# Optimization experiments

Hardware: AMD Instinct MI355X
Metric: run time of the kernel (lower is better)

The kernel has to match this reference:

```python
import jax, jax.numpy as jnp
import numpy as np

# ---- static skeleton topology (20 edges, humanoid: spine + 2 arms + 2 legs) ----
EDGES = [(0,1),(1,2),(2,3),(3,4),(3,5),(5,6),(6,7),(7,8),(3,9),(9,10),(10,11),(11,12),
         (0,13),(13,14),(14,15),(15,16),(0,17),(17,18),(18,19),(19,20)]
SKELETON_DIST = 2
IN_PER_J, OUT_PER_J = 64, 128
KSIZE, PAD, STRIDE = 15, 7, 2
BATCH, T = 8, 4096


def _calc_edge_mat(edges):
    n = len(edges)
    INF = 100000
    m = np.full((n, n), INF, dtype=np.int64)
    np.fill_diagonal(m, 0)
    for i, a in enumerate(edges):
        for j, b in enumerate(edges):
            if a[0] in b or a[1] in b:
                m[i, j] = min(m[i, j], 1)
    for k in range(n):  # Floyd-Warshall on tiny static graph
        m = np.minimum(m, m[:, k:k+1] + m[k:k+1, :])
    return m


def _find_neighbor(edges, d):
    m = _calc_edge_mat(edges)
    n = len(edges)
    neigh = [[j for j in range(n) if m[i, j] <= d] for i in range(n)]
    global_part = list(neigh[0])
    for i in global_part:
        neigh[i].append(n)  # virtual global edge index n
    neigh.append(global_part)
    return neigh


def _build_mask(neigh, in_pj, out_pj, k):
    J = len(neigh)
    mask = np.zeros((J * out_pj, J * in_pj, k), dtype=np.float32)
    for i, nb in enumerate(neigh):
        for j in nb:
            mask[i*out_pj:(i+1)*out_pj, j*in_pj:(j+1)*in_pj, :] = 1.0
    return mask


def _build_pool_weight(edges, cpe):
    degree = [0] * 100
    for e in edges:
        degree[e[0]] += 1
        degree[e[1]] += 1
    seq_list = []
    def find_seq(j, seq):
        if degree[j] > 2 and j != 0:
            seq_list.append(seq); seq = []
        if degree[j] == 1:
            seq_list.append(seq); return
        for idx, e in enumerate(edges):
            if e[0] == j:
                find_seq(e[1], seq + [idx])
    find_seq(0, [])
    pooling = []
    for seq in seq_list:
        seq = list(seq)
        if len(seq) % 2 == 1:
            pooling.append([seq[0]]); seq = seq[1:]
        for i in range(0, len(seq), 2):
            pooling.append([seq[i], seq[i+1]])
    edge_num = len(edges) + 1
    pooling.append([edge_num - 1])
    W = np.zeros((len(pooling) * cpe, edge_num * cpe), dtype=np.float32)
    for i, pair in enumerate(pooling):
        for j in pair:
            for c in range(cpe):
                W[i*cpe + c, j*cpe + c] = 1.0 / len(pair)
    return W


def setup_inputs() -> dict:
    key = jax.random.key(0)
    k1, k2, k3 = jax.random.split(key, 3)
    J = len(EDGES) + 1  # 21 (edges + virtual global)
    in_c, out_c = J * IN_PER_J, J * OUT_PER_J  # 1344, 2688
    neigh = _find_neighbor(EDGES, SKELETON_DIST)
    mask = jnp.asarray(_build_mask(neigh, IN_PER_J, OUT_PER_J, KSIZE))
    pool_w = jnp.asarray(_build_pool_weight(EDGES, out_c // J))
    x = jax.random.normal(k1, (BATCH, in_c, T), dtype=jnp.float32)
    weight = jax.random.normal(k2, (out_c, in_c, KSIZE), dtype=jnp.float32) * 0.02
    bias = jax.random.normal(k3, (out_c,), dtype=jnp.float32) * 0.01
    return {"x": x, "weight": weight, "bias": bias, "mask": mask, "pool_w": pool_w}


def reference(x, weight, bias, mask, pool_w):
    # SkeletonConv: per-joint neighbor mask applied to dense conv1d weights
    w = weight * mask  # [out_c, in_c, K]
    xp = jnp.pad(x, ((0, 0), (0, 0), (PAD, PAD)), mode='reflect')
    y = jax.lax.conv_general_dilated(
        xp, w, window_strides=(STRIDE,), padding='VALID',
        dimension_numbers=('NCH', 'OIH', 'NCH'))
    y = y + bias[None, :, None]  # [B, out_c, T//2]
    # SkeletonPool: mean over graph-defined edge groups via matmul
    p = jnp.einsum('pc,bct->bpt', pool_w, y)
    # LeakyReLU activation as in the layer stack
    return jax.nn.leaky_relu(p, negative_slope=0.2)
```

## Files before the change

kernel.cpp:

```cpp
#include <hip/hip_runtime.h>
#include <cstdint>
#include <cstddef>

typedef unsigned short u16;
typedef unsigned int   u32;

typedef __bf16 bf16x8 __attribute__((ext_vector_type(8)));
typedef float  f32x4  __attribute__((ext_vector_type(4)));

#define AS1C(p) ((const __attribute__((address_space(1))) void*)(p))
#define AS3(p)  ((__attribute__((address_space(3))) void*)(p))

__constant__ int d_slot_jb[85] = {
  0,1,2,12,13,16,17,20,
  0,1,2,3,4,5,8,9,12,16,20,
  1,2,3,4,5,8,9,
  1,2,3,4,5,6,7,8,9,
  4,5,6,7,
  1,2,3,4,5,8,9,10,11,
  8,9,10,11,
  0,1,12,13,14,15,16,17,20,
  12,13,14,15,
  0,1,12,13,16,17,18,19,20,
  16,17,18,19,
  0,1,2,12,13,16,17
};
__constant__ int   d_gs0[12]    = {0,8,19,26,35,39,48,52,61,65,74,78};
__constant__ int   d_gnb[12]    = {8,11,7,9,4,9,4,9,4,9,4,7};
__constant__ int   d_gj0[12]    = {0,1,3,4,6,8,10,12,14,16,18,20};
__constant__ int   d_gj1[12]    = {-1,2,-1,5,7,9,11,13,15,17,19,-1};
__constant__ float d_gscale[12] = {1.f,0.5f,1.f,0.5f,0.5f,0.5f,0.5f,0.5f,0.5f,0.5f,0.5f,1.f};
__constant__ int   d_sched[12]  = {1,3,5,7,9,0,2,11,4,6,8,10};

static __device__ __forceinline__ u16 f2bf(float f) {
  union { float f; u32 u; } v; v.f = f;
  u32 r = v.u + 0x7fffu + ((v.u >> 16) & 1u);
  return (u16)(r >> 16);
}

__global__ void prep_x(const float* __restrict__ x, u16* __restrict__ xp) {
  int gid = blockIdx.x * 256 + threadIdx.x;
  if (gid >= 8 * 1344 * 514) return;
  int pc  = gid % 514;
  int row = gid / 514;
  int p   = pc * 8;
  const float* xr = x + (size_t)row * 4096;
  u16 v[8];
#pragma unroll
  for (int e = 0; e < 8; ++e) {
    int j = p + e - 7;
    j = j < 0 ? -j : (j > 4095 ? 8190 - j : j);
    v[e] = f2bf(xr[j]);
  }
  *(uint4*)(xp + (size_t)row * 4112 + p) = *(const uint4*)v;
}

__global__ void prep_w(const float* __restrict__ wt, const float* __restrict__ msk,
                       u16* __restrict__ apk) {
  int gid = blockIdx.x * 256 + threadIdx.x;
  if (gid >= 85 * 8192) return;
  int u   = gid >> 13;
  int rem = gid & 8191;
  int m   = rem >> 6;
  int c   = rem & 63;
  int g = 11;
#pragma unroll
  for (int gg = 0; gg < 11; ++gg)
    if (u >= d_gs0[gg] && u < d_gs0[gg + 1]) g = gg;
  int jb = d_slot_jb[u];
  int j0 = d_gj0[g], j1 = d_gj1[g];
  float sc = d_gscale[g];
  float m0 = msk[((size_t)(j0 * 128) * 1344 + jb * 64) * 15];
  float m1 = (j1 >= 0) ? msk[((size_t)(j1 * 128) * 1344 + jb * 64) * 15] : 0.f;
  const float* w0 = wt + ((size_t)(j0 * 128 + m) * 1344 + jb * 64 + c) * 15;
  const float* w1 = (j1 >= 0) ? wt + ((size_t)(j1 * 128 + m) * 1344 + jb * 64 + c) * 15 : w0;
  u16 v[16];
#pragma unroll
  for (int k = 0; k < 15; ++k) {
    float a = m0 * w0[k] + m1 * w1[k];
    v[k] = f2bf(a * sc);
  }
  v[15] = 0;
  uint4* dst = (uint4*)(apk + (size_t)u * 131072 + m * 1024 + c * 16);
  dst[0] = ((const uint4*)v)[0];
  dst[1] = ((const uint4*)v)[1];
}

__global__ void prep_b(const float* __restrict__ bias, float* __restrict__ bg) {
  int pc = blockIdx.x * 256 + threadIdx.x;
  if (pc >= 1536) return;
  int g = pc >> 7, m = pc & 127;
  float v = bias[d_gj0[g] * 128 + m];
  if (d_gj1[g] >= 0) v += bias[d_gj1[g] * 128 + m];
  bg[pc] = v * d_gscale[g];
}

__global__ __launch_bounds__(256, 3)
void conv_main(const u16* __restrict__ xpbf, const u16* __restrict__ apk,
               const float* __restrict__ biasg, float* __restrict__ out) {
  __shared__ __align__(16) u16 xs[64 * 280];
  __shared__ __align__(16) u16 as[128 * 64];

  const int tid = threadIdx.x;
  const int l   = tid & 63, w = tid >> 6;
  const int q   = l >> 4, lm = l & 15;
  const int wm  = w & 1, wn = w >> 1;

  const int gidx = blockIdx.x >> 7;
  const int g    = d_sched[gidx];
  const int r    = blockIdx.x & 127;
  const int b    = r >> 4;
  const int tile = r & 15;
  const int t0   = tile << 7;
  const int p0   = t0 << 1;

  const int nb = d_gnb[g];
  const int s0 = d_gs0[g];

  f32x4 acc[4][4];
#pragma unroll
  for (int i = 0; i < 4; ++i)
#pragma unroll
    for (int j = 0; j < 4; ++j)
      acc[i][j] = (f32x4){0.f, 0.f, 0.f, 0.f};

  const int as_mb = tid >> 3;
  const int as_sp = tid & 7;

  for (int s = 0; s < nb; ++s) {
    const int u  = s0 + s;
    const int jb = d_slot_jb[u];
    __syncthreads();
    {
      const u16* srow = xpbf + (size_t)(b * 1344 + jb * 64) * 4112 + p0;
      for (int i = tid; i < 64 * 34; i += 256) {
        int c  = i / 34;
        int sg = i - c * 34;
        uint4 v = *(const uint4*)(srow + (size_t)c * 4112 + sg * 8);
        *(uint4*)((char*)xs + c * 560 + sg * 16) = v;
      }
    }
    const u16* ablk = apk + (size_t)u * 131072;
    for (int kc = 0; kc < 16; ++kc) {
      __syncthreads();
#pragma unroll
      for (int ii = 0; ii < 4; ++ii) {
        int m    = ii * 32 + as_mb;
        int sloc = as_sp ^ (m & 7);
        const u16* gp = ablk + m * 1024 + kc * 64 + sloc * 8;
        __builtin_amdgcn_global_load_lds(AS1C(gp),
                                         AS3((char*)as + ii * 4096 + w * 1024),
                                         16, 0, 0);
      }
      __syncthreads();
#pragma unroll
      for (int ks = 0; ks < 2; ++ks) {
        bf16x8 af[4];
#pragma unroll
        for (int mt = 0; mt < 4; ++mt) {
          int m  = wm * 64 + mt * 16 + lm;
          int sp = (ks * 4 + q) ^ (m & 7);
          af[mt] = *(const bf16x8*)((const char*)as + m * 128 + sp * 16);
        }
        const int crow = kc * 4 + ks * 2 + (q >> 1);
        const char* xrow = (const char*)xs + crow * 560 + 16 * (q & 1);
#pragma unroll
        for (int nt = 0; nt < 4; ++nt) {
          int n = wn * 64 + nt * 16 + lm;
          const char* bp = xrow + 4 * n;
          union { u32 u[4]; bf16x8 v; } bb;
#pragma unroll
          for (int ww = 0; ww < 4; ++ww)
            bb.u[ww] = *(const u32*)(bp + 4 * ww);
#pragma unroll
          for (int mt = 0; mt < 4; ++mt)
            acc[mt][nt] = __builtin_amdgcn_mfma_f32_16x16x32_bf16(
                af[mt], bb.v, acc[mt][nt], 0, 0, 0);
        }
      }
    }
  }

  const float* bgp = biasg + g * 128 + wm * 64;
  float* outb = out + ((size_t)b * 1536 + g * 128 + wm * 64) * 2048 + t0 + wn * 64;
#pragma unroll
  for (int mt = 0; mt < 4; ++mt) {
    const f32x4 bv = *(const f32x4*)(bgp + mt * 16 + q * 4);
#pragma unroll
    for (int reg = 0; reg < 4; ++reg) {
      const float bias = bv[reg];
      const int m = mt * 16 + q * 4 + reg;
      float* orow = outb + (size_t)m * 2048 + lm;
#pragma unroll
      for (int nt = 0; nt < 4; ++nt) {
        float v = acc[mt][nt][reg] + bias;
        orow[nt * 16] = v < 0.f ? 0.2f * v : v;
      }
    }
  }
}

extern "C" void kernel_launch(void* const* d_in, const int* in_sizes, int n_in,
                              void* d_out, int out_size, void* d_ws, size_t ws_size,
                              hipStream_t stream) {
  (void)in_sizes; (void)n_in; (void)out_size; (void)ws_size;
  const float* x   = (const float*)d_in[0];
  const float* wt  = (const float*)d_in[1];
  const float* bs  = (const float*)d_in[2];
  const float* msk = (const float*)d_in[3];

  u16*   xpbf = (u16*)d_ws;
  u16*   apk  = (u16*)((char*)d_ws + 88424448);
  float* bg   = (float*)((char*)d_ws + 110706688);
  float* out  = (float*)d_out;

  prep_x<<<dim3(21588), dim3(256), 0, stream>>>(x, xpbf);
  prep_w<<<dim3(2720),  dim3(256), 0, stream>>>(wt, msk, apk);
  prep_b<<<dim3(6),     dim3(256), 0, stream>>>(bs, bg);
  conv_main<<<dim3(1536), dim3(256), 0, stream>>>(xpbf, apk, bg, out);
}
```

Before: 782.3 us.

## Load weight fragments directly from global into registers with double buffering

```diff
diff --git a/kernel.cpp b/kernel.cpp
--- a/kernel.cpp
+++ b/kernel.cpp
@@ -7,9 +7,6 @@
 
 typedef __bf16 bf16x8 __attribute__((ext_vector_type(8)));
 typedef float  f32x4  __attribute__((ext_vector_type(4)));
-
-#define AS1C(p) ((const __attribute__((address_space(1))) void*)(p))
-#define AS3(p)  ((__attribute__((address_space(3))) void*)(p))
 
 __constant__ int d_slot_jb[85] = {
   0,1,2,12,13,16,17,20,
@@ -81,7 +78,7 @@
     v[k] = f2bf(a * sc);
   }
   v[15] = 0;
-  uint4* dst = (uint4*)(apk + (size_t)u * 131072 + m * 1024 + c * 16);
+  uint4* dst = (uint4*)(apk + (size_t)u * 131072 + (c >> 1) * 4096 + m * 32 + (c & 1) * 16);
   dst[0] = ((const uint4*)v)[0];
   dst[1] = ((const uint4*)v)[1];
 }
@@ -95,11 +92,30 @@
   bg[pc] = v * d_gscale[g];
 }
 
+static __device__ __forceinline__ void load_a(bf16x8 dst[4], const u16* __restrict__ p) {
+#pragma unroll
+  for (int mt = 0; mt < 4; ++mt)
+    dst[mt] = *(const bf16x8*)(p + mt * 512);
+}
+
+static __device__ __forceinline__ void compute_chunk(
+    const bf16x8 af[4], const u32* __restrict__ xr32, int c32, f32x4 acc[4][4]) {
+#pragma unroll
+  for (int nt = 0; nt < 4; ++nt) {
+    union { u32 u[4]; bf16x8 v; } bb;
+#pragma unroll
+    for (int ww = 0; ww < 4; ++ww)
+      bb.u[ww] = xr32[c32 * 280 + nt * 16 + ww];
+#pragma unroll
+    for (int mt = 0; mt < 4; ++mt)
+      acc[mt][nt] = __builtin_amdgcn_mfma_f32_16x16x32_bf16(af[mt], bb.v, acc[mt][nt], 0, 0, 0);
+  }
+}
+
 __global__ __launch_bounds__(256, 3)
 void conv_main(const u16* __restrict__ xpbf, const u16* __restrict__ apk,
                const float* __restrict__ biasg, float* __restrict__ out) {
   __shared__ __align__(16) u16 xs[64 * 280];
-  __shared__ __align__(16) u16 as[128 * 64];
 
   const int tid = threadIdx.x;
   const int l   = tid & 63, w = tid >> 6;
@@ -124,8 +140,10 @@
     for (int j = 0; j < 4; ++j)
       acc[i][j] = (f32x4){0.f, 0.f, 0.f, 0.f};
 
-  const int as_mb = tid >> 3;
-  const int as_sp = tid & 7;
+  const int a_off = (wm * 64 + lm) * 32 + q * 8;
+  const u32* xr32 = (const u32*)(xs + (q >> 1) * 280 + (q & 1) * 8 + (wn * 64 + lm) * 2);
+
+  bf16x8 afA[4], afB[4];
 
   for (int s = 0; s < nb; ++s) {
     const int u  = s0 + s;
@@ -140,44 +158,17 @@
         *(uint4*)((char*)xs + c * 560 + sg * 16) = v;
       }
     }
-    const u16* ablk = apk + (size_t)u * 131072;
-    for (int kc = 0; kc < 16; ++kc) {
-      __syncthreads();
-#pragma unroll
-      for (int ii = 0; ii < 4; ++ii) {
-        int m    = ii * 32 + as_mb;
-        int sloc = as_sp ^ (m & 7);
-        const u16* gp = ablk + m * 1024 + kc * 64 + sloc * 8;
-        __builtin_amdgcn_global_load_lds(AS1C(gp),
-                                         AS3((char*)as + ii * 4096 + w * 1024),
-                                         16, 0, 0);
-      }
-      __syncthreads();
-#pragma unroll
-      for (int ks = 0; ks < 2; ++ks) {
-        bf16x8 af[4];
-#pragma unroll
-        for (int mt = 0; mt < 4; ++mt) {
-          int m  = wm * 64 + mt * 16 + lm;
-          int sp = (ks * 4 + q) ^ (m & 7);
-          af[mt] = *(const bf16x8*)((const char*)as + m * 128 + sp * 16);
-        }
-        const int crow = kc * 4 + ks * 2 + (q >> 1);
-        const char* xrow = (const char*)xs + crow * 560 + 16 * (q & 1);
-#pragma unroll
-        for (int nt = 0; nt < 4; ++nt) {
-          int n = wn * 64 + nt * 16 + lm;
-          const char* bp = xrow + 4 * n;
-          union { u32 u[4]; bf16x8 v; } bb;
-#pragma unroll
-          for (int ww = 0; ww < 4; ++ww)
-            bb.u[ww] = *(const u32*)(bp + 4 * ww);
-#pragma unroll
-          for (int mt = 0; mt < 4; ++mt)
-            acc[mt][nt] = __builtin_amdgcn_mfma_f32_16x16x32_bf16(
-                af[mt], bb.v, acc[mt][nt], 0, 0, 0);
-        }
-      }
+    __syncthreads();
+
+    const u16* ap = apk + (size_t)u * 131072 + a_off;
+    load_a(afA, ap);
+#pragma unroll
+    for (int k2 = 0; k2 < 16; ++k2) {
+      load_a(afB, ap + 4096);
+      compute_chunk(afA, xr32, 2 * k2, acc);
+      if (k2 < 15) load_a(afA, ap + 8192);
+      compute_chunk(afB, xr32, 2 * k2 + 1, acc);
+      ap += 8192;
     }
   }
 
```

Result: slower. 874.1 us (+11.7%).
